# Performance work log

Hardware: AMD Instinct MI355X
Metric: run time of the kernel (lower is better)

Reference implementation:

```python
import jax, jax.numpy as jnp
import numpy as np

B, C, T = 16, 64, 4096
K1, O1 = 3, 2
K2, O2 = 5, 2
D = O1 + O2  # total dendritic paths per channel
DEC = 128
TAU, THRESH = 5.0, 1.0
ALPHA = float(np.exp(-1.0 / TAU))


def setup_inputs() -> dict:
    key = jax.random.key(0)
    ks = jax.random.split(key, 14)

    def unif(k, shape, fan_in):  # torch conv/linear default init
        b = 1.0 / np.sqrt(fan_in)
        return jax.random.uniform(k, shape, minval=-b, maxval=b, dtype=jnp.float32)

    x = jax.random.normal(ks[0], (B, C, T), dtype=jnp.float32)
    # depthwise convs: torch weight (C*out_per, 1, k), group-major channel order
    w3 = unif(ks[1], (C * O1, 1, K1), K1)
    b3 = unif(ks[2], (C * O1,), K1)
    w5 = unif(ks[3], (C * O2, 1, K2), K2)
    b5 = unif(ks[4], (C * O2,), K2)
    # reduce: Conv1d(C*D -> C, k=1, groups=C) => weight (C, D)
    reduce_w = unif(ks[5], (C, D), D)
    reduce_b = unif(ks[6], (C,), D)
    latency_scale = jnp.asarray(5.0, dtype=jnp.float32)
    # xavier uniform on (C,C), diagonal zeroed
    xb = float(np.sqrt(6.0 / (C + C)))
    output_gates = jax.random.uniform(ks[7], (C, C), minval=-xb, maxval=xb, dtype=jnp.float32)
    output_gates = output_gates * (1.0 - jnp.eye(C, dtype=jnp.float32))
    mlp_w1 = unif(ks[8], (DEC, C), C)
    mlp_b1 = unif(ks[9], (DEC,), C)
    mlp_w2 = unif(ks[10], (C, DEC), DEC)
    mlp_b2 = unif(ks[11], (C,), DEC)
    return {"x": x, "w3": w3, "b3": b3, "w5": w5, "b5": b5,
            "reduce_w": reduce_w, "reduce_b": reduce_b,
            "latency_scale": latency_scale, "output_gates": output_gates,
            "mlp_w1": mlp_w1, "mlp_b1": mlp_b1, "mlp_w2": mlp_w2, "mlp_b2": mlp_b2}


def _dwconv(x, w, b, k):
    # depthwise grouped conv, 'same' padding, groups=C
    pad = (k - 1) // 2
    y = jax.lax.conv_general_dilated(
        x, w, window_strides=(1,), padding=[(pad, pad)],
        dimension_numbers=("NCH", "OIH", "NCH"), feature_group_count=C)
    return y + b[None, :, None]


def _forward(x, w3, b3, w5, b5, reduce_w, reduce_b,
             latency_scale, output_gates, mlp_w1, mlp_b1, mlp_w2, mlp_b2):
    # encoder: multi-path depthwise convs -> dendritic_drive (B,C,D,T)
    o3 = _dwconv(x, w3, b3, K1).reshape(B, C, O1, T)
    o5 = _dwconv(x, w5, b5, K2).reshape(B, C, O2, T)
    dendritic_drive = jnp.concatenate([o3, o5], axis=2)  # (B,C,D,T)
    # grouped 1x1 reduce: per-channel mix over D
    summed = jnp.einsum("bcdt,cd->bct", dendritic_drive, reduce_w) + reduce_b[None, :, None]

    # LIF latency: leaky integrate over T, first-crossing time (T if none)
    def step(V, d_t):
        V = ALPHA * V + (1.0 - ALPHA) * d_t
        return V, V >= THRESH

    _, spikes = jax.lax.scan(step, jnp.zeros((B, C), dtype=summed.dtype),
                             jnp.moveaxis(summed, 2, 0))  # spikes: (T,B,C) bool
    any_fired = spikes.any(axis=0)
    first_t = jnp.argmax(spikes, axis=0)  # first True index
    true_latency = jnp.where(any_fired, first_t, T).astype(summed.dtype)  # (B,C)

    scale = jnp.maximum(latency_scale, 0.001)
    act = jnp.exp(-true_latency / scale)  # (B,C)
    mixed = act @ output_gates.T
    h = jax.nn.relu(mixed @ mlp_w1.T + mlp_b1)
    raw_pred = h @ mlp_w2.T + mlp_b2
    pred_latency = jnp.clip(jax.nn.softplus(raw_pred), 0.0, float(T))
    return pred_latency, true_latency, act, dendritic_drive


def reference(x, w3, b3, w5, b5, reduce_w, reduce_b,
              latency_scale, output_gates, mlp_w1, mlp_b1, mlp_w2, mlp_b2):
    return _forward(x, w3, b3, w5, b5, reduce_w, reduce_b,
                    latency_scale, output_gates, mlp_w1, mlp_b1, mlp_w2, mlp_b2)
```

## Files before the change

kernel.cpp:

```cpp
#include <hip/hip_runtime.h>
#include <math.h>

#define NB 16
#define NC 64
#define NT 4096
#define NDEC 128

#define ALPHA_F 0.81873075307798185867f
#define ONEMA_F 0.18126924692201814133f
#define Q16_F   0.040762203978366216f

#define LGKM_BARRIER() asm volatile("s_waitcnt lgkmcnt(0)\n\ts_barrier" ::: "memory")

__global__ __launch_bounds__(256) void conv_lif_kernel(
    const float* __restrict__ x,
    const float* __restrict__ w3, const float* __restrict__ b3,
    const float* __restrict__ w5, const float* __restrict__ b5,
    const float* __restrict__ rw, const float* __restrict__ rb,
    float* __restrict__ out)
{
    __shared__ __align__(16) float s_x[4 + NT + 4];
    __shared__ float s_sum[NT + 256];
    __shared__ float s_part[4];
    __shared__ int   s_wmin[4];

    const int bc  = blockIdx.x;
    const int c   = bc & (NC - 1);
    const int tid = threadIdx.x;
    const int lane = tid & 63;

    if (tid < 4) { s_x[tid] = 0.f; s_x[4 + NT + tid] = 0.f; }
    {
        const float4* x4  = (const float4*)(x + (size_t)bc * NT);
        float4*       sx4 = (float4*)(s_x + 4);
        #pragma unroll
        for (int i = 0; i < 4; ++i) sx4[i * 256 + tid] = x4[i * 256 + tid];
    }

    const float w30a = w3[(c*2+0)*3+0], w30b = w3[(c*2+0)*3+1], w30c = w3[(c*2+0)*3+2];
    const float w31a = w3[(c*2+1)*3+0], w31b = w3[(c*2+1)*3+1], w31c = w3[(c*2+1)*3+2];
    const float b30 = b3[c*2+0], b31 = b3[c*2+1];
    const float* w50p = w5 + (c*2+0)*5;
    const float* w51p = w5 + (c*2+1)*5;
    const float w50a=w50p[0], w50b=w50p[1], w50c=w50p[2], w50d=w50p[3], w50e=w50p[4];
    const float w51a=w51p[0], w51b=w51p[1], w51c=w51p[2], w51d=w51p[3], w51e=w51p[4];
    const float b50 = b5[c*2+0], b51 = b5[c*2+1];
    const float rw0 = rw[c*4+0], rw1 = rw[c*4+1], rw2 = rw[c*4+2], rw3 = rw[c*4+3];
    const float rbc = rb[c];

    __syncthreads();

    float* dd = out + 3072 + (size_t)bc * (4 * NT);
    #pragma unroll
    for (int i = 0; i < 4; ++i) {
        const int t = i * 1024 + tid * 4;
        const float4 c0 = *(const float4*)(s_x + t);
        const float4 c1 = *(const float4*)(s_x + t + 4);
        const float4 c2 = *(const float4*)(s_x + t + 8);
        const float in[8] = {c0.z, c0.w, c1.x, c1.y, c1.z, c1.w, c2.x, c2.y};
        float4 v30, v31, v50, v51;
        const int pad = t >> 4;
        #pragma unroll
        for (int j = 0; j < 4; ++j) {
            const float xm2 = in[j], xm1 = in[j+1], x0 = in[j+2];
            const float xp1 = in[j+3], xp2 = in[j+4];
            float o30 = fmaf(w30c, xp1, fmaf(w30b, x0, fmaf(w30a, xm1, b30)));
            float o31 = fmaf(w31c, xp1, fmaf(w31b, x0, fmaf(w31a, xm1, b31)));
            float o50 = fmaf(w50e, xp2, fmaf(w50d, xp1, fmaf(w50c, x0,
                        fmaf(w50b, xm1, fmaf(w50a, xm2, b50)))));
            float o51 = fmaf(w51e, xp2, fmaf(w51d, xp1, fmaf(w51c, x0,
                        fmaf(w51b, xm1, fmaf(w51a, xm2, b51)))));
            ((float*)&v30)[j] = o30;
            ((float*)&v31)[j] = o31;
            ((float*)&v50)[j] = o50;
            ((float*)&v51)[j] = o51;
            s_sum[t + j + pad] = fmaf(rw3, o51, fmaf(rw2, o50,
                                 fmaf(rw1, o31, fmaf(rw0, o30, rbc))));
        }
        *(float4*)(dd + t)          = v30;
        *(float4*)(dd + NT + t)     = v31;
        *(float4*)(dd + 2 * NT + t) = v50;
        *(float4*)(dd + 3 * NT + t) = v51;
    }
    LGKM_BARRIER();

    const int t0 = tid * 16;
    float dv[16];
    #pragma unroll
    for (int j = 0; j < 16; ++j) dv[j] = s_sum[t0 + tid + j];

    float V = 0.f;
    #pragma unroll
    for (int j = 0; j < 16; ++j)
        V = __fadd_rn(__fmul_rn(ALPHA_F, V), __fmul_rn(ONEMA_F, dv[j]));

    float S = V;
    float coef = Q16_F;
    #pragma unroll
    for (int off = 1; off <= 16; off <<= 1) {
        float p = __shfl_up(S, off);
        if (lane >= off) S = fmaf(coef, p, S);
        coef *= coef;
    }

    if (lane == 63) s_part[tid >> 6] = S;
    LGKM_BARRIER();
    const float Pprev = (tid >= 64) ? s_part[(tid >> 6) - 1] : 0.f;

    float ql = 1.f, qp = Q16_F;
    #pragma unroll
    for (int bit = 0; bit < 6; ++bit) {
        if ((lane >> bit) & 1) ql *= qp;
        qp *= qp;
    }

    float Sm1 = __shfl_up(S, 1);
    float V2 = fmaf(Pprev, ql, (lane > 0) ? Sm1 : 0.f);
    int firstt = NT;
    #pragma unroll
    for (int j = 0; j < 16; ++j) {
        V2 = __fadd_rn(__fmul_rn(ALPHA_F, V2), __fmul_rn(ONEMA_F, dv[j]));
        if (V2 >= 1.0f && firstt == NT) firstt = t0 + j;
    }

    int m = firstt;
    #pragma unroll
    for (int off = 32; off > 0; off >>= 1) m = min(m, __shfl_down(m, off));
    if (lane == 0) s_wmin[tid >> 6] = m;
    LGKM_BARRIER();
    if (tid == 0) {
        int r = min(min(s_wmin[0], s_wmin[1]), min(s_wmin[2], s_wmin[3]));
        out[1024 + bc] = (float)r;
    }
}

__global__ __launch_bounds__(128) void head_kernel(
    const float* __restrict__ lat_scale,
    const float* __restrict__ og,
    const float* __restrict__ w1, const float* __restrict__ b1,
    const float* __restrict__ w2, const float* __restrict__ b2,
    float* __restrict__ out)
{
    __shared__ float act_s[NC];
    __shared__ float mixed_s[NC];
    __shared__ float h_s[NDEC];
    const int b   = blockIdx.x;
    const int tid = threadIdx.x;
    const float scale = fmaxf(lat_scale[0], 0.001f);

    if (tid < NC) {
        float tl = out[1024 + b * NC + tid];
        float a  = expf(-tl / scale);
        act_s[tid] = a;
        out[2048 + b * NC + tid] = a;
    }
    __syncthreads();

    if (tid < NC) {
        float mx = 0.f;
        #pragma unroll 8
        for (int cc = 0; cc < NC; ++cc) mx = fmaf(act_s[cc], og[tid * NC + cc], mx);
        mixed_s[tid] = mx;
    }
    __syncthreads();

    {
        float h = b1[tid];
        #pragma unroll 8
        for (int i = 0; i < NC; ++i) h = fmaf(mixed_s[i], w1[tid * NC + i], h);
        h_s[tid] = fmaxf(h, 0.f);
    }
    __syncthreads();

    if (tid < NC) {
        float r = b2[tid];
        #pragma unroll 8
        for (int j = 0; j < NDEC; ++j) r = fmaf(h_s[j], w2[tid * NDEC + j], r);
        float sp = fmaxf(r, 0.f) + log1pf(expf(-fabsf(r)));
        out[b * NC + tid] = fminf(sp, (float)NT);
    }
}

extern "C" void kernel_launch(void* const* d_in, const int* in_sizes, int n_in,
                              void* d_out, int out_size, void* d_ws, size_t ws_size,
                              hipStream_t stream) {
    const float* x  = (const float*)d_in[0];
    const float* w3 = (const float*)d_in[1];
    const float* b3 = (const float*)d_in[2];
    const float* w5 = (const float*)d_in[3];
    const float* b5 = (const float*)d_in[4];
    const float* rw = (const float*)d_in[5];
    const float* rb = (const float*)d_in[6];
    const float* ls = (const float*)d_in[7];
    const float* og = (const float*)d_in[8];
    const float* w1 = (const float*)d_in[9];
    const float* b1 = (const float*)d_in[10];
    const float* w2 = (const float*)d_in[11];
    const float* b2 = (const float*)d_in[12];
    float* out = (float*)d_out;

    conv_lif_kernel<<<NB * NC, 256, 0, stream>>>(x, w3, b3, w5, b5, rw, rb, out);
    head_kernel<<<NB, 128, 0, stream>>>(ls, og, w1, b1, w2, b2, out);
}
```

Measured before the change: 113.9 us.

## Fuse MLP head into conv/LIF kernel via last-block atomic counter

Removes the separate head kernel launch. Each block writes its latency and activation, then bumps a global atomic counter, and the last block to finish computes the gate mix, MLP and softplus for all batches. This saves one kernel launch and its gap, but adds a hipMemsetAsync for the counter and runs the whole head serially on a single block at the end. It also relies on the global reads from the last block seeing the other blocks' writes.

```diff
diff --git a/kernel.cpp b/kernel.cpp
--- a/kernel.cpp
+++ b/kernel.cpp
@@ -12,17 +12,22 @@
 
 #define LGKM_BARRIER() asm volatile("s_waitcnt lgkmcnt(0)\n\ts_barrier" ::: "memory")
 
-__global__ __launch_bounds__(256) void conv_lif_kernel(
+__global__ __launch_bounds__(256) void conv_lif_fused(
     const float* __restrict__ x,
     const float* __restrict__ w3, const float* __restrict__ b3,
     const float* __restrict__ w5, const float* __restrict__ b5,
     const float* __restrict__ rw, const float* __restrict__ rb,
-    float* __restrict__ out)
+    const float* __restrict__ lat_scale,
+    const float* __restrict__ og,
+    const float* __restrict__ w1, const float* __restrict__ b1,
+    const float* __restrict__ w2, const float* __restrict__ b2,
+    float* __restrict__ out, int* __restrict__ counter)
 {
     __shared__ __align__(16) float s_x[4 + NT + 4];
     __shared__ float s_sum[NT + 256];
     __shared__ float s_part[4];
     __shared__ int   s_wmin[4];
+    __shared__ int   s_is_last;
 
     const int bc  = blockIdx.x;
     const int c   = bc & (NC - 1);
@@ -128,56 +133,67 @@
     for (int off = 32; off > 0; off >>= 1) m = min(m, __shfl_down(m, off));
     if (lane == 0) s_wmin[tid >> 6] = m;
     LGKM_BARRIER();
+
     if (tid == 0) {
         int r = min(min(s_wmin[0], s_wmin[1]), min(s_wmin[2], s_wmin[3]));
-        out[1024 + bc] = (float)r;
-    }
-}
-
-__global__ __launch_bounds__(128) void head_kernel(
-    const float* __restrict__ lat_scale,
-    const float* __restrict__ og,
-    const float* __restrict__ w1, const float* __restrict__ b1,
-    const float* __restrict__ w2, const float* __restrict__ b2,
-    float* __restrict__ out)
-{
-    __shared__ float act_s[NC];
-    __shared__ float mixed_s[NC];
-    __shared__ float h_s[NDEC];
-    const int b   = blockIdx.x;
-    const int tid = threadIdx.x;
+        float tl = (float)r;
+        out[1024 + bc] = tl;
+        const float scale = fmaxf(lat_scale[0], 0.001f);
+        out[2048 + bc] = expf(-tl / scale);
+        int prev = __hip_atomic_fetch_add(counter, 1, __ATOMIC_ACQ_REL,
+                                          __HIP_MEMORY_SCOPE_AGENT);
+        s_is_last = (prev == (int)(NB * NC) - 1);
+    }
+    __syncthreads();
+    if (!s_is_last) return;
+
+    float* s_act   = s_x;
+    float* s_mixed = s_x + 1024;
+    float* s_h     = s_sum;
+
     const float scale = fmaxf(lat_scale[0], 0.001f);
 
-    if (tid < NC) {
-        float tl = out[1024 + b * NC + tid];
-        float a  = expf(-tl / scale);
-        act_s[tid] = a;
-        out[2048 + b * NC + tid] = a;
-    }
-    __syncthreads();
-
-    if (tid < NC) {
+    #pragma unroll
+    for (int k = tid; k < 1024; k += 256) {
+        float tl = out[1024 + k];
+        s_act[k] = expf(-tl / scale);
+    }
+    __syncthreads();
+
+    #pragma unroll
+    for (int k = tid; k < 1024; k += 256) {
+        int b = k >> 6, cc0 = k & 63;
+        const float* ob = og + cc0 * NC;
+        const float* ab = s_act + b * NC;
         float mx = 0.f;
         #pragma unroll 8
-        for (int cc = 0; cc < NC; ++cc) mx = fmaf(act_s[cc], og[tid * NC + cc], mx);
-        mixed_s[tid] = mx;
-    }
-    __syncthreads();
-
-    {
-        float h = b1[tid];
+        for (int cc = 0; cc < NC; ++cc) mx = fmaf(ab[cc], ob[cc], mx);
+        s_mixed[k] = mx;
+    }
+    __syncthreads();
+
+    #pragma unroll
+    for (int k = tid; k < 2048; k += 256) {
+        int b = k >> 7, j = k & 127;
+        const float* mb = s_mixed + b * NC;
+        const float* wj = w1 + j * NC;
+        float h = b1[j];
         #pragma unroll 8
-        for (int i = 0; i < NC; ++i) h = fmaf(mixed_s[i], w1[tid * NC + i], h);
-        h_s[tid] = fmaxf(h, 0.f);
-    }
-    __syncthreads();
-
-    if (tid < NC) {
-        float r = b2[tid];
+        for (int i = 0; i < NC; ++i) h = fmaf(mb[i], wj[i], h);
+        s_h[k] = fmaxf(h, 0.f);
+    }
+    __syncthreads();
+
+    #pragma unroll
+    for (int k = tid; k < 1024; k += 256) {
+        int b = k >> 6, cc0 = k & 63;
+        const float* hb = s_h + b * NDEC;
+        const float* wc = w2 + cc0 * NDEC;
+        float r = b2[cc0];
         #pragma unroll 8
-        for (int j = 0; j < NDEC; ++j) r = fmaf(h_s[j], w2[tid * NDEC + j], r);
+        for (int j = 0; j < NDEC; ++j) r = fmaf(hb[j], wc[j], r);
         float sp = fmaxf(r, 0.f) + log1pf(expf(-fabsf(r)));
-        out[b * NC + tid] = fminf(sp, (float)NT);
+        out[k] = fminf(sp, (float)NT);
     }
 }
 
@@ -198,7 +214,9 @@
     const float* w2 = (const float*)d_in[11];
     const float* b2 = (const float*)d_in[12];
     float* out = (float*)d_out;
-
-    conv_lif_kernel<<<NB * NC, 256, 0, stream>>>(x, w3, b3, w5, b5, rw, rb, out);
-    head_kernel<<<NB, 128, 0, stream>>>(ls, og, w1, b1, w2, b2, out);
+    int* counter = (int*)d_ws;
+
+    hipMemsetAsync(counter, 0, sizeof(int), stream);
+    conv_lif_fused<<<NB * NC, 256, 0, stream>>>(
+        x, w3, b3, w5, b5, rw, rb, ls, og, w1, b1, w2, b2, out, counter);
 }
```

Result: slower. 181.3 us (+59.2%).
